# Kernel tuning notes

Measured on AMD Instinct MI355X. Metric: run time of the kernel, lower is better.

The kernel has to match this reference:

```python
import jax, jax.numpy as jnp
import numpy as np

PATCH = 288
DIM = 2048
SCALE = DIM ** -0.5
NUM_INSTANCE = 4
B, Q, H, W = 32, 16, 24, 12


def _layernorm(x):
    # elementwise_affine=False LayerNorm, eps=1e-5
    m = jnp.mean(x, axis=-1, keepdims=True)
    v = jnp.mean((x - m) ** 2, axis=-1, keepdims=True)
    return (x - m) / jnp.sqrt(v + 1e-5)


def _l2norm(x):
    n = jnp.sqrt(jnp.sum(x * x, axis=-1, keepdims=True))
    return x / jnp.maximum(n, 1e-12)


def _catcher(x, g, cam_embed, Wq, Wg, pos_embed):
    # x: [B,Q,C] queries; g: [B,N,C] tokens; cam_embed: [B*N//PATCH,1,C] or None
    rel_q = jnp.einsum('bqc,dc->bqd', x, Wq)
    Bg, N, C = g.shape
    G = Bg * N // PATCH
    g2 = g.reshape(G, PATCH, C)
    rel = _l2norm(g2)
    rel = jax.nn.softmax(jnp.einsum('gpc,gqc->gpq', rel, rel), axis=-1)
    g2 = jnp.einsum('gpq,gqc->gpc', rel, g2)  # [G,PATCH,C]
    if cam_embed is not None:
        rel_g = g2 + cam_embed.reshape(G, 1, C)  # cam embed replaces pos embed (as in torch)
    else:
        rel_g = g2 + pos_embed
    g_out = g2.reshape(Bg, N, C)
    rel_g = jnp.einsum('bnc,dc->bnd', rel_g.reshape(Bg, N, C), Wg)
    att = jax.nn.softmax(jnp.einsum('bqc,bnc->bqn', rel_q, rel_g) * SCALE, axis=-1)
    out = jnp.einsum('bqn,bnc->bqc', att, g_out)
    return out, att


def _deltaor(x, g, Wq, Wg):
    q = _layernorm(x)
    rel_q = jnp.einsum('bqc,dc->bqd', q, Wq)
    g = g - jnp.mean(x, axis=1, keepdims=True)
    g = _layernorm(g)
    rel_g = jnp.einsum('bnc,dc->bnd', g, Wg)
    att = jax.nn.softmax(jnp.einsum('bqc,bnc->bqn', rel_q, rel_g) * SCALE, axis=-1)
    return x + jnp.einsum('bqn,bnc->bqc', att, g)


def setup_inputs() -> dict:
    key = jax.random.key(0)
    ks = jax.random.split(key, 12)
    w_scale = DIM ** -0.5
    return {
        'x': jax.random.normal(ks[0], (B, DIM, H, W), dtype=jnp.float32),
        'cam_ids': jax.random.randint(ks[1], (B,), 1, 7),
        'sub': jax.random.randint(ks[2], (B,), 0, 2).astype(bool),
        'query_v': 0.02 * jax.random.normal(ks[3], (1, Q, DIM), dtype=jnp.float32),
        'prototype': 0.02 * jax.random.normal(ks[4], (1, 2048, DIM), dtype=jnp.float32),
        'weights': jnp.ones((1, Q, 1), dtype=jnp.float32),
        'cam_table': 0.02 * jax.random.normal(ks[5], (6, 1, DIM), dtype=jnp.float32),
        'pos_embed': 0.02 * jax.random.normal(ks[6], (1, PATCH, DIM), dtype=jnp.float32),
        'Wcq': w_scale * jax.random.normal(ks[7], (DIM, DIM), dtype=jnp.float32),
        'Wcg': w_scale * jax.random.normal(ks[8], (DIM, DIM), dtype=jnp.float32),
        'Wdq': w_scale * jax.random.normal(ks[9], (DIM, DIM), dtype=jnp.float32),
        'Wdg': w_scale * jax.random.normal(ks[10], (DIM, DIM), dtype=jnp.float32),
    }


def reference(x, cam_ids, sub, query_v, prototype, weights, cam_table, pos_embed,
              Wcq, Wcg, Wdq, Wdg):
    Bx, C, Hx, Wx = x.shape
    HW = Hx * Wx
    xs = jnp.transpose(x.reshape(Bx, C, HW), (0, 2, 1))  # [B,HW,C]
    query = jnp.broadcast_to(query_v, (Bx,) + query_v.shape[1:])
    proto = jnp.broadcast_to(prototype, (Bx,) + prototype.shape[1:])
    cam_embed = cam_table[cam_ids - 1]  # [B,1,C]

    f_rel, _ = _catcher(query, xs, cam_embed, Wcq, Wcg, pos_embed)
    f_pro = _deltaor(f_rel, proto, Wdq, Wdg)

    # training branch (P2R shares weights with Q2R)
    f_rec, _ = _catcher(f_pro, xs, cam_embed, Wcq, Wcg, pos_embed)

    G = Bx // NUM_INSTANCE
    ce = cam_embed.reshape(G, 1, NUM_INSTANCE, 1, C)
    ce = jnp.broadcast_to(ce, (G, NUM_INSTANCE, NUM_INSTANCE, 1, C)).reshape(Bx, NUM_INSTANCE, C)
    xr = xs.reshape(G, 1, NUM_INSTANCE, HW, C)
    xr = jnp.broadcast_to(xr, (G, NUM_INSTANCE, NUM_INSTANCE, HW, C)).reshape(Bx, NUM_INSTANCE * HW, C)
    # torch.cat([a[~sub], a[sub]]) == stable sort by sub (False first)
    perm = jnp.argsort(sub.astype(jnp.int32))
    ce = ce[perm]
    xr = xr[perm]
    f_cor, _ = _catcher(f_pro, xr, ce, Wcq, Wcg, pos_embed)

    f_pro = jax.nn.softmax(weights, axis=1) * f_pro
    return f_rel, f_pro, f_rec, f_cor
```

## Files before the change

### kernel.cpp

```cpp
#include <hip/hip_runtime.h>
#include <math.h>

static constexpr float SCALE = 0.022097086912079612f;

typedef __bf16 bf16x4 __attribute__((ext_vector_type(4)));
typedef __bf16 bf16x8 __attribute__((ext_vector_type(8)));
typedef float  f32x4  __attribute__((ext_vector_type(4)));

__device__ __forceinline__ float wred_sum(float v){
  #pragma unroll
  for (int o=32;o>0;o>>=1) v += __shfl_down(v,o,64);
  return v;
}
__device__ __forceinline__ float wred_max(float v){
  #pragma unroll
  for (int o=32;o>0;o>>=1) v = fmaxf(v, __shfl_down(v,o,64));
  return v;
}
__device__ __forceinline__ float block_sum(float v, float* red){
  int tid=threadIdx.x, w=tid>>6, l=tid&63, nw=(int)(blockDim.x>>6);
  v = wred_sum(v);
  __syncthreads();
  if (l==0) red[w]=v;
  __syncthreads();
  float r=0.f;
  for (int i=0;i<nw;i++) r += red[i];
  return r;
}
__device__ __forceinline__ float block_max(float v, float* red){
  int tid=threadIdx.x, w=tid>>6, l=tid&63, nw=(int)(blockDim.x>>6);
  v = wred_max(v);
  __syncthreads();
  if (l==0) red[w]=v;
  __syncthreads();
  float r=red[0];
  for (int i=1;i<nw;i++) r = fmaxf(r, red[i]);
  return r;
}

template<int MT, int NT, int WM, int WN>
__global__ __launch_bounds__(256, 2)
void gemm_nt_mfma(float* __restrict__ Cm, const float* __restrict__ Am,
                  const float* __restrict__ Bm, int M, int N, int K,
                  int lda, int ldb, int ldc, long sA, long sB, long sC,
                  float alpha, const int* __restrict__ browidx, long sBrow,
                  int KS, float* __restrict__ Part)
{
  constexpr int BM = MT*16*WM;
  constexpr int BN = NT*16*WN;
  constexpr int LDH = 40;
  constexpr int AST = (BM+31)/32;
  constexpr int BST = (BN+31)/32;
  __shared__ __bf16 Ah[BM*LDH];
  __shared__ __bf16 Al[BM*LDH];
  __shared__ __bf16 Bh[BN*LDH];
  __shared__ __bf16 Bl[BN*LDH];
  int ZZ = gridDim.z / KS;
  int z  = blockIdx.z % ZZ;
  int ks = blockIdx.z / ZZ;
  const float* A = Am + (long)z*sA;
  const float* B = Bm + (long)z*sB;
  float* C = Cm + (long)z*sC;
  const bool useB = (browidx != nullptr);
  const int* brow = useB ? (browidx + (long)z*sBrow) : nullptr;
  int Kc = ((K + KS*32 - 1) / (KS*32)) * 32;
  int kbeg = ks*Kc;
  int kend = min(K, kbeg + Kc);
  int m0 = blockIdx.y*BM, n0 = blockIdx.x*BN;
  int t = threadIdx.x;
  int srow = t>>3, skoff = (t&7)*4;

  float4 areg[AST], breg[BST];
  auto loadAB = [&](int k0){
    #pragma unroll
    for (int s=0;s<AST;++s){
      int row = srow + 32*s; int gm = m0+row;
      areg[s] = make_float4(0.f,0.f,0.f,0.f);
      if (row < BM && gm < M) areg[s] = *(const float4*)(A + (long)gm*lda + k0 + skoff);
    }
    #pragma unroll
    for (int s=0;s<BST;++s){
      int row = srow + 32*s; int gn = n0+row;
      breg[s] = make_float4(0.f,0.f,0.f,0.f);
      if (row < BN && gn < N){
        long r = useB ? (long)brow[gn] : (long)gn;
        breg[s] = *(const float4*)(B + r*ldb + k0 + skoff);
      }
    }
  };
  auto writeLDS = [&](){
    #pragma unroll
    for (int s=0;s<AST;++s){
      int row = srow + 32*s;
      if (row < BM){
        float vv[4] = {areg[s].x, areg[s].y, areg[s].z, areg[s].w};
        bf16x4 hv, lv;
        #pragma unroll
        for (int e=0;e<4;++e){
          __bf16 h = (__bf16)vv[e];
          hv[e] = h;
          lv[e] = (__bf16)(vv[e] - (float)h);
        }
        *(bf16x4*)&Ah[row*LDH + skoff] = hv;
        *(bf16x4*)&Al[row*LDH + skoff] = lv;
      }
    }
    #pragma unroll
    for (int s=0;s<BST;++s){
      int row = srow + 32*s;
      if (row < BN){
        float vv[4] = {breg[s].x, breg[s].y, breg[s].z, breg[s].w};
        bf16x4 hv, lv;
        #pragma unroll
        for (int e=0;e<4;++e){
          __bf16 h = (__bf16)vv[e];
          hv[e] = h;
          lv[e] = (__bf16)(vv[e] - (float)h);
        }
        *(bf16x4*)&Bh[row*LDH + skoff] = hv;
        *(bf16x4*)&Bl[row*LDH + skoff] = lv;
      }
    }
  };

  int lane = t & 63, wid = t >> 6;
  int wm = (WM==1) ? 0 : (wid / WN);
  int wn = wid % WN;
  int mw = wm*MT*16, nw = wn*NT*16;
  int fr = lane & 15, fq = (lane>>4)*8;

  f32x4 acc[MT][NT];
  #pragma unroll
  for (int i=0;i<MT;++i)
    #pragma unroll
    for (int j=0;j<NT;++j) acc[i][j] = (f32x4){0.f,0.f,0.f,0.f};

  if (kbeg < kend) loadAB(kbeg);
  for (int k0=kbeg; k0<kend; k0+=32){
    writeLDS();
    __syncthreads();
    if (k0+32 < kend) loadAB(k0+32);
    bf16x8 ah[MT], al[MT], bh[NT], bl[NT];
    #pragma unroll
    for (int i=0;i<MT;++i){
      ah[i] = *(const bf16x8*)&Ah[(mw+i*16+fr)*LDH + fq];
      al[i] = *(const bf16x8*)&Al[(mw+i*16+fr)*LDH + fq];
    }
    #pragma unroll
    for (int j=0;j<NT;++j){
      bh[j] = *(const bf16x8*)&Bh[(nw+j*16+fr)*LDH + fq];
      bl[j] = *(const bf16x8*)&Bl[(nw+j*16+fr)*LDH + fq];
    }
    #pragma unroll
    for (int i=0;i<MT;++i)
      #pragma unroll
      for (int j=0;j<NT;++j){
        acc[i][j] = __builtin_amdgcn_mfma_f32_16x16x32_bf16(ah[i], bh[j], acc[i][j], 0,0,0);
        acc[i][j] = __builtin_amdgcn_mfma_f32_16x16x32_bf16(ah[i], bl[j], acc[i][j], 0,0,0);
        acc[i][j] = __builtin_amdgcn_mfma_f32_16x16x32_bf16(al[i], bh[j], acc[i][j], 0,0,0);
      }
    __syncthreads();
  }
  float wf = (KS==1) ? alpha : 1.f;
  float* Cw = C; int ldw = ldc;
  if (ks > 0){ Cw = Part + ((long)(ks-1)*ZZ + z)*(long)M*N; ldw = N; }
  int er = (lane>>4)*4, ec = lane & 15;
  #pragma unroll
  for (int i=0;i<MT;++i){
    int mbase = m0 + mw + i*16 + er;
    #pragma unroll
    for (int r=0;r<4;++r){
      int mm = mbase + r;
      if (mm < M){
        long cro = (long)mm*ldw;
        #pragma unroll
        for (int j=0;j<NT;++j){
          int nn = n0 + nw + j*16 + ec;
          if (nn < N) Cw[cro + nn] = wf*acc[i][j][r];
        }
      }
    }
  }
}

template<int MT, int NT, int WM, int WN>
__global__ __launch_bounds__(256, 2)
void gemm_nt_bs(float* __restrict__ C,
                const __bf16* __restrict__ Ahg, const __bf16* __restrict__ Alg,
                const __bf16* __restrict__ Bhg, const __bf16* __restrict__ Blg,
                int M, int N, int K, int lda, int ldb, int ldc,
                float alpha, int KS, float* __restrict__ Part)
{
  constexpr int BM = MT*16*WM;
  constexpr int BN = NT*16*WN;
  constexpr int LDH = 40;
  __shared__ __bf16 Ah[BM*LDH];
  __shared__ __bf16 Al[BM*LDH];
  __shared__ __bf16 Bh[BN*LDH];
  __shared__ __bf16 Bl[BN*LDH];
  int ks = blockIdx.z;
  int Kc = ((K + KS*32 - 1) / (KS*32)) * 32;
  int kbeg = ks*Kc;
  int kend = min(K, kbeg + Kc);
  int m0 = blockIdx.y*BM, n0 = blockIdx.x*BN;
  int t = threadIdx.x;
  constexpr int ASl = (BM*4 + 255)/256;
  constexpr int BSl = (BN*4 + 255)/256;
  bf16x8 arh[ASl], arl[ASl], brh[BSl], brl[BSl];
  bf16x8 zed;
  #pragma unroll
  for (int e=0;e<8;++e) zed[e] = (__bf16)0.f;

  auto loadAB = [&](int k0){
    #pragma unroll
    for (int i=0;i<ASl;++i){
      int s = t + 256*i;
      arh[i] = zed; arl[i] = zed;
      if (s < BM*4){
        int row = s>>2, koff = (s&3)*8; int gm = m0+row;
        if (gm < M){
          long off = (long)gm*lda + k0 + koff;
          arh[i] = *(const bf16x8*)(Ahg + off);
          arl[i] = *(const bf16x8*)(Alg + off);
        }
      }
    }
    #pragma unroll
    for (int i=0;i<BSl;++i){
      int s = t + 256*i;
      brh[i] = zed; brl[i] = zed;
      if (s < BN*4){
        int row = s>>2, koff = (s&3)*8; int gn = n0+row;
        if (gn < N){
          long off = (long)gn*ldb + k0 + koff;
          brh[i] = *(const bf16x8*)(Bhg + off);
          brl[i] = *(const bf16x8*)(Blg + off);
        }
      }
    }
  };
  auto writeLDS = [&](){
    #pragma unroll
    for (int i=0;i<ASl;++i){
      int s = t + 256*i;
      if (s < BM*4){
        int row = s>>2, koff = (s&3)*8;
        *(bf16x8*)&Ah[row*LDH + koff] = arh[i];
        *(bf16x8*)&Al[row*LDH + koff] = arl[i];
      }
    }
    #pragma unroll
    for (int i=0;i<BSl;++i){
      int s = t + 256*i;
      if (s < BN*4){
        int row = s>>2, koff = (s&3)*8;
        *(bf16x8*)&Bh[row*LDH + koff] = brh[i];
        *(bf16x8*)&Bl[row*LDH + koff] = brl[i];
      }
    }
  };

  int lane = t & 63, wid = t >> 6;
  int wm = (WM==1) ? 0 : (wid / WN);
  int wn = wid % WN;
  int mw = wm*MT*16, nw = wn*NT*16;
  int fr = lane & 15, fq = (lane>>4)*8;

  f32x4 acc[MT][NT];
  #pragma unroll
  for (int i=0;i<MT;++i)
    #pragma unroll
    for (int j=0;j<NT;++j) acc[i][j] = (f32x4){0.f,0.f,0.f,0.f};

  if (kbeg < kend) loadAB(kbeg);
  for (int k0=kbeg; k0<kend; k0+=32){
    writeLDS();
    __syncthreads();
    if (k0+32 < kend) loadAB(k0+32);
    bf16x8 ah[MT], al[MT], bh[NT], bl[NT];
    #pragma unroll
    for (int i=0;i<MT;++i){
      ah[i] = *(const bf16x8*)&Ah[(mw+i*16+fr)*LDH + fq];
      al[i] = *(const bf16x8*)&Al[(mw+i*16+fr)*LDH + fq];
    }
    #pragma unroll
    for (int j=0;j<NT;++j){
      bh[j] = *(const bf16x8*)&Bh[(nw+j*16+fr)*LDH + fq];
      bl[j] = *(const bf16x8*)&Bl[(nw+j*16+fr)*LDH + fq];
    }
    #pragma unroll
    for (int i=0;i<MT;++i)
      #pragma unroll
      for (int j=0;j<NT;++j){
        acc[i][j] = __builtin_amdgcn_mfma_f32_16x16x32_bf16(ah[i], bh[j], acc[i][j], 0,0,0);
        acc[i][j] = __builtin_amdgcn_mfma_f32_16x16x32_bf16(ah[i], bl[j], acc[i][j], 0,0,0);
        acc[i][j] = __builtin_amdgcn_mfma_f32_16x16x32_bf16(al[i], bh[j], acc[i][j], 0,0,0);
      }
    __syncthreads();
  }
  float wf = (KS==1) ? alpha : 1.f;
  float* Cw = C; int ldw = ldc;
  if (ks > 0){ Cw = Part + (long)(ks-1)*(long)M*N; ldw = N; }
  int er = (lane>>4)*4, ec = lane & 15;
  #pragma unroll
  for (int i=0;i<MT;++i){
    int mbase = m0 + mw + i*16 + er;
    #pragma unroll
    for (int r=0;r<4;++r){
      int mm = mbase + r;
      if (mm < M){
        long cro = (long)mm*ldw;
        #pragma unroll
        for (int j=0;j<NT;++j){
          int nn = n0 + nw + j*16 + ec;
          if (nn < N) Cw[cro + nn] = wf*acc[i][j][r];
        }
      }
    }
  }
}

__global__ __launch_bounds__(256) void k_reduce(float* __restrict__ C, const float* __restrict__ Part,
                                                long total, int S, float alpha){
  for (long i = (long)blockIdx.x*blockDim.x + threadIdx.x; i < total;
       i += (long)gridDim.x*blockDim.x){
    float v = C[i];
    for (int s=0;s<S;++s) v += Part[(long)s*total + i];
    C[i] = alpha*v;
  }
}

__global__ __launch_bounds__(256) void k_reduce_split(float* __restrict__ C, const float* __restrict__ Part,
                                                      long total, int S, float alpha,
                                                      __bf16* __restrict__ H, __bf16* __restrict__ L){
  long n4 = total >> 2;
  for (long i = (long)blockIdx.x*blockDim.x + threadIdx.x; i < n4;
       i += (long)gridDim.x*blockDim.x){
    float4 v = ((float4*)C)[i];
    for (int s=0;s<S;++s){
      float4 p = ((const float4*)(Part + (long)s*total))[i];
      v.x += p.x; v.y += p.y; v.z += p.z; v.w += p.w;
    }
    v.x *= alpha; v.y *= alpha; v.z *= alpha; v.w *= alpha;
    ((float4*)C)[i] = v;
    float vv[4] = {v.x, v.y, v.z, v.w};
    bf16x4 h, l;
    #pragma unroll
    for (int e=0;e<4;++e){
      __bf16 hh = (__bf16)vv[e];
      h[e] = hh;
      l[e] = (__bf16)(vv[e] - (float)hh);
    }
    ((bf16x4*)H)[i] = h;
    ((bf16x4*)L)[i] = l;
  }
}

__global__ __launch_bounds__(256) void k_split(const float* __restrict__ X,
                                               __bf16* __restrict__ H, __bf16* __restrict__ L, long n){
  long n4 = n >> 2;
  for (long i = (long)blockIdx.x*blockDim.x + threadIdx.x; i < n4;
       i += (long)gridDim.x*blockDim.x){
    float4 v = ((const float4*)X)[i];
    float vv[4] = {v.x, v.y, v.z, v.w};
    bf16x4 h, l;
    #pragma unroll
    for (int e=0;e<4;++e){
      __bf16 hh = (__bf16)vv[e];
      h[e] = hh;
      l[e] = (__bf16)(vv[e] - (float)hh);
    }
    ((bf16x4*)H)[i] = h;
    ((bf16x4*)L)[i] = l;
  }
}

__global__ __launch_bounds__(256, 2) void k_pv(
    float* __restrict__ C, float* __restrict__ Part,
    const float* __restrict__ Pm, long sP, int K, int Kc,
    const float* __restrict__ G, long sG, const int* __restrict__ SB)
{
  extern __shared__ float Pl[];
  int b = blockIdx.y, ks = blockIdx.z;
  int kbeg = ks * Kc;
  int kend = min(K, kbeg + Kc);
  int len = kend - kbeg;
  int c0 = blockIdx.x*1024 + threadIdx.x*4;
  const float* Pb = Pm + (long)b*sP;
  for (int i = threadIdx.x; i < 16*len; i += 256){
    int q = i / len, kk = i - q*len;
    Pl[q*Kc + kk] = Pb[(long)q*K + kbeg + kk];
  }
  __syncthreads();
  f32x4 acc[16];
  #pragma unroll
  for (int q=0;q<16;++q) acc[q] = (f32x4){0.f,0.f,0.f,0.f};
  int kk = 0;
  while (kk < len){
    int kg = kbeg + kk;
    int seg = kg / 288;
    int row = kg - seg*288;
    int nrow = min(288 - row, len - kk);
    const float* gp = (SB ? (G + (long)SB[(b<<2)+seg]*sG) : (G + (long)b*sG))
                      + (long)row*2048 + c0;
    for (int r = 0; r < nrow; r += 4, kk += 4){
      f32x4 g0 = *(const f32x4*)(gp);
      f32x4 g1 = *(const f32x4*)(gp + 2048);
      f32x4 g2 = *(const f32x4*)(gp + 4096);
      f32x4 g3 = *(const f32x4*)(gp + 6144);
      gp += 8192;
      #pragma unroll
      for (int q=0;q<16;++q){
        f32x4 p = *(const f32x4*)&Pl[q*Kc + kk];
        acc[q] += p[0]*g0;
        acc[q] += p[1]*g1;
        acc[q] += p[2]*g2;
        acc[q] += p[3]*g3;
      }
    }
  }
  float* Cw = (ks==0) ? C : (Part + (long)(ks-1)*1048576);
  long obase = (long)b*32768 + c0;
  #pragma unroll
  for (int q=0;q<16;++q) *(f32x4*)&Cw[obase + (long)q*2048] = acc[q];
}

__global__ void k_tr(const float* __restrict__ in, float* __restrict__ out, int R, int C){
  __shared__ float tile[32][33];
  long zo = (long)blockIdx.z * R * C;
  int r0 = blockIdx.y*32, c0 = blockIdx.x*32;
  int tx = threadIdx.x, ty = threadIdx.y;
  #pragma unroll
  for (int j=0;j<32;j+=8)
    tile[ty+j][tx] = in[zo + (long)(r0+ty+j)*C + c0+tx];
  __syncthreads();
  #pragma unroll
  for (int j=0;j<32;j+=8)
    out[zo + (long)(c0+ty+j)*R + r0+tx] = tile[tx][ty+j];
}

__global__ void k_tr_split(const float* __restrict__ in, __bf16* __restrict__ oh,
                           __bf16* __restrict__ ol, int R, int C){
  __shared__ float tile[32][33];
  int r0 = blockIdx.y*32, c0 = blockIdx.x*32;
  int tx = threadIdx.x, ty = threadIdx.y;
  #pragma unroll
  for (int j=0;j<32;j+=8)
    tile[ty+j][tx] = in[(long)(r0+ty+j)*C + c0+tx];
  __syncthreads();
  #pragma unroll
  for (int j=0;j<32;j+=8){
    float v = tile[tx][ty+j];
    __bf16 h = (__bf16)v;
    long idx = (long)(c0+ty+j)*R + r0+tx;
    oh[idx] = h;
    ol[idx] = (__bf16)(v - (float)h);
  }
}

__global__ __launch_bounds__(256) void k_rowstats(const float* __restrict__ X, long ldx, int cols,
                                                  float* __restrict__ mu, float* __restrict__ m2){
  int r = blockIdx.x;
  const float* row = X + (long)r*ldx;
  float s=0.f, s2=0.f;
  for (int c = threadIdx.x*4; c < cols; c += 1024){
    float4 v = *(const float4*)(row+c);
    s  += v.x+v.y+v.z+v.w;
    s2 += v.x*v.x+v.y*v.y+v.z*v.z+v.w*v.w;
  }
  __shared__ float red[8];
  s  = block_sum(s,  red);
  s2 = block_sum(s2, red);
  if (threadIdx.x==0){ mu[r]=s/(float)cols; m2[r]=s2; }
}

__global__ __launch_bounds__(256) void k_softmax_gram(float* __restrict__ S, const float* __restrict__ Part,
                                                      const float* __restrict__ m2xs){
  int r = blockIdx.x;
  int b = r / 288, p = r % 288;
  float* row = S + (long)r * 288;
  const float* prow = Part + (long)b*82944 + (long)p*288;
  const float* m2 = m2xs + (long)b*288;
  float rp = 1.f / fmaxf(sqrtf(m2[p]), 1e-12f);
  int tid = threadIdx.x;
  __shared__ float red[8];
  float lv[2];
  #pragma unroll
  for (int i=0;i<2;++i){
    int q = tid + i*256;
    lv[i] = (q<288) ? (row[q]+prow[q])*rp/fmaxf(sqrtf(m2[q]),1e-12f) : -1e30f;
  }
  float mx = fmaxf(lv[0], lv[1]);
  mx = block_max(mx, red);
  float s = 0.f;
  #pragma unroll
  for (int i=0;i<2;++i){
    int q = tid + i*256;
    float e = (q<288) ? expf(lv[i]-mx) : 0.f;
    lv[i]=e; s+=e;
  }
  s = block_sum(s, red);
  float inv = 1.f/s;
  #pragma unroll
  for (int i=0;i<2;++i){ int q = tid + i*256; if (q<288) row[q]=lv[i]*inv; }
}

__global__ __launch_bounds__(256) void k_softmax_plain_r(float* __restrict__ X,
// ... 111 lines not shown
  int r = blockIdx.x; int b = r >> 4;
  const float* a = relq2 + (long)r*2048;
  const float* m = Mx + (long)b*2048;
  float s=0.f, sw=0.f;
  for (int c = threadIdx.x*4; c < 2048; c += 1024){
    float4 va=*(const float4*)(a+c), vm=*(const float4*)(m+c), vw=*(const float4*)(muw+c);
    s  += va.x*vm.x+va.y*vm.y+va.z*vm.z+va.w*vm.w;
    sw += va.x*vw.x+va.y*vw.y+va.z*vw.z+va.w*vw.w;
  }
  __shared__ float red[8];
  s  = block_sum(s,  red);
  sw = block_sum(sw, red);
  if (threadIdx.x==0){ qm[r]=s; qw[r]=sw; }
}

__global__ __launch_bounds__(256) void k_score2_s(const float* __restrict__ QPw, const float* __restrict__ qm,
                                                  const float* __restrict__ qw,
                                                  const float* __restrict__ sigma, const float* __restrict__ mu_p,
                                                  __bf16* __restrict__ QH, __bf16* __restrict__ QL,
                                                  float* __restrict__ W1, float* __restrict__ Wmu, float scale){
  int r = blockIdx.x; int b = r >> 4;
  const float* row = QPw + (long)r*2048;
  const float* sg = sigma + (long)b*2048;
  int tid = threadIdx.x;
  __shared__ float red[8];
  float qmr = qm[r];
  float qwr2048 = 2048.f * qw[r];
  float lv[8], ls[8], lmp[8];
  #pragma unroll
  for (int i=0;i<8;++i){
    int n = tid + i*256;
    float sgn = sg[n];
    float mpn = mu_p[n];
    ls[i] = sgn;
    lmp[i] = mpn;
    lv[i] = scale * (row[n] - qwr2048*mpn - qmr) / sgn;
  }
  float mx = -1e30f;
  #pragma unroll
  for (int i=0;i<8;++i) mx = fmaxf(mx, lv[i]);
  mx = block_max(mx, red);
  float se=0.f, sw=0.f, swm=0.f;
  #pragma unroll
  for (int i=0;i<8;++i){
    float e = expf(lv[i]-mx);
    lv[i] = e; se += e;
    float wv = e/ls[i];
    sw += wv; swm += wv*lmp[i];
  }
  se  = block_sum(se,  red);
  sw  = block_sum(sw,  red);
  swm = block_sum(swm, red);
  float inv = 1.f/se;
  #pragma unroll
  for (int i=0;i<8;++i){
    int n = tid + i*256;
    float v = lv[i]*inv/ls[i];
    __bf16 h = (__bf16)v;
    long idx = (long)r*2048 + n;
    QH[idx] = h;
    QL[idx] = (__bf16)(v - (float)h);
  }
  if (tid==0){ W1[r]=sw*inv; Wmu[r]=swm*inv; }
}

__global__ void k_fpro_final_s(const float* __restrict__ frel, const float* __restrict__ out2,
                               const float* __restrict__ meanx, const float* __restrict__ mu_m,
                               const float* __restrict__ W1, const float* __restrict__ Wmu,
                               const float* __restrict__ wsm,
                               __bf16* __restrict__ FH, __bf16* __restrict__ FL,
                               float* __restrict__ fout){
  int r = blockIdx.y; int c = blockIdx.x*256 + threadIdx.x;
  int b = r >> 4, q = r & 15;
  long idx = (long)r*2048 + c;
  float w1 = W1[r];
  float v = frel[idx] + out2[idx] - meanx[(long)b*2048+c]*w1 - Wmu[r] + mu_m[b]*w1;
  __bf16 h = (__bf16)v;
  FH[idx] = h;
  FL[idx] = (__bf16)(v - (float)h);
  fout[idx] = wsm[q] * v;
}

__global__ void k_camb(const float* __restrict__ cam_table, const int* __restrict__ cam_ids,
                       float* __restrict__ camb){
  int b = blockIdx.y; int c = blockIdx.x*256 + threadIdx.x;
  camb[(long)b*2048 + c] = cam_table[(long)(cam_ids[b]-1)*2048 + c];
}

__global__ void k_wsoft(const float* __restrict__ w, float* __restrict__ wsm){
  if (threadIdx.x==0){
    float mx=-1e30f;
    for (int i=0;i<16;++i) mx=fmaxf(mx,w[i]);
    float e[16], s=0.f;
    for (int i=0;i<16;++i){ e[i]=expf(w[i]-mx); s+=e[i]; }
    for (int i=0;i<16;++i) wsm[i]=e[i]/s;
  }
}

__global__ void k_perm(const void* __restrict__ subp, int* __restrict__ gidx, int* __restrict__ SB){
  __shared__ int perm[32];
  if (threadIdx.x==0){
    const int* pi = (const int*)subp;
    const float* pf = (const float*)subp;
    const unsigned char* pb = (const unsigned char*)subp;
    int sv[32]; bool okI=true, okF=true;
    for (int i=0;i<32;++i){ int v=pi[i]; if (v!=0 && v!=1) okI=false; }
    for (int i=0;i<32;++i){ float f=pf[i]; if (f!=0.f && f!=1.f) okF=false; }
    for (int i=0;i<32;++i){
      if (okI) sv[i]=pi[i];
      else if (okF) sv[i]=(pf[i]!=0.f)?1:0;
      else sv[i]=(pb[i]!=0)?1:0;
    }
    int pos=0;
    for (int i=0;i<32;++i) if (!sv[i]) perm[pos++]=i;
    for (int i=0;i<32;++i) if ( sv[i]) perm[pos++]=i;
  }
  __syncthreads();
  for (int i = threadIdx.x; i < 128; i += blockDim.x){
    int b = i>>2, j = i&3;
    SB[i] = ((perm[b]>>2)<<2) + j;
  }
  for (int idx = threadIdx.x; idx < 32*1152; idx += blockDim.x){
    int b = idx / 1152, rem = idx % 1152, j = rem / 288, n = rem % 288;
    int src = ((perm[b] >> 2) << 2) + j;
    gidx[idx] = src*288 + n;
  }
}

extern "C" void kernel_launch(void* const* d_in, const int* in_sizes, int n_in,
                              void* d_out, int out_size, void* d_ws, size_t ws_size,
                              hipStream_t stream) {
  const float* x        = (const float*)d_in[0];
  const int*   cam_ids  = (const int*)d_in[1];
  const void*  subp     = d_in[2];
  const float* query_v  = (const float*)d_in[3];
  const float* proto    = (const float*)d_in[4];
  const float* weights  = (const float*)d_in[5];
  const float* cam_tab  = (const float*)d_in[6];
  const float* Wcq      = (const float*)d_in[8];
  const float* Wcg      = (const float*)d_in[9];
  const float* Wdq      = (const float*)d_in[10];
  const float* Wdg      = (const float*)d_in[11];
  float* out = (float*)d_out;
  float* ws  = (float*)d_ws;

  size_t o = 0;
  float* S     = ws + o; o += 2654208;
  __bf16* QLNh   = (__bf16*)S;
  __bf16* QLNl   = (__bf16*)(S + 524288);
  __bf16* RELQ2h = (__bf16*)(S + 1048576);
  __bf16* RELQ2l = (__bf16*)(S + 1572864);
  float* XSR   = ws + o; o += 18874368;
  float* XS    = XSR;
  float* PART  = XSR;
  __bf16* WCQh  = (__bf16*)(XSR + 6291456);
  __bf16* WCQl  = (__bf16*)(XSR + 8388608);
  __bf16* WCGTh = (__bf16*)(XSR + 10485760);
  __bf16* WCGTl = (__bf16*)(XSR + 12582912);
  __bf16* ROTh  = (__bf16*)(XSR + 14680064);
  __bf16* ROTl  = (__bf16*)(XSR + 16777216);
  float* GMIX  = ws + o; o += 18874368;
  float* MU_XS = ws + o; o += 9216;
  float* M2_XS = ws + o; o += 9216;
  float* CAMB  = ws + o; o += 65536;
  float* RQ0   = ws + o; o += 32768;
  float* RQW   = ws + o; o += 32768;
  float* SREL  = ws + o; o += 147456;
  float* MU_FR = ws + o; o += 512;
  float* M2_FR = ws + o; o += 512;
  float* T1    = ws + o; o += 1048576;
  float* RELQ2 = ws + o; o += 1048576;
  float* MEANX = ws + o; o += 65536;
  float* MU_P  = ws + o; o += 2048;
  float* M2_P  = ws + o; o += 2048;
  float* MU_M  = ws + o; o += 64;
  float* M2_M  = ws + o; o += 64;
  float* MU_W  = ws + o; o += 2048;
  float* M2_W  = ws + o; o += 2048;
  float* PM    = ws + o; o += 65536;
  float* SIGMA = ws + o; o += 65536;
  float* MX    = ws + o; o += 65536;
  float* QP    = ws + o; o += 1048576;
  float* QM    = ws + o; o += 512;
  float* QW    = ws + o; o += 512;
  float* W1    = ws + o; o += 512;
  float* WMU   = ws + o; o += 512;
  float* OUT2  = ws + o; o += 1048576;
  __bf16* FPROh = (__bf16*)(ws + o);
  __bf16* FPROl = (__bf16*)(ws + o + 524288); o += 1048576;
  float* RQ2   = ws + o; o += 1048576;
  float* RQW2  = ws + o; o += 1048576;
  float* SREC  = ws + o; o += 147456;
  float* SCOR  = ws + o; o += 589824;
  float* CC    = ws + o; o += 16384;
  float* WSM   = ws + o; o += 16;
  __bf16* T1h   = (__bf16*)(ws + o);
  __bf16* T1l   = (__bf16*)(ws + o + 524288); o += 1048576;
  __bf16* QPWh  = (__bf16*)(ws + o);
  __bf16* QPWl  = (__bf16*)(ws + o + 524288); o += 1048576;
  __bf16* RQ2h  = (__bf16*)(ws + o);
  __bf16* RQ2l  = (__bf16*)(ws + o + 524288); o += 1048576;
  __bf16* QVh   = (__bf16*)(ws + o);
  __bf16* QVl   = (__bf16*)(ws + o + 16384); o += 32768;
  __bf16* RQ0h  = (__bf16*)(ws + o);
  __bf16* RQ0l  = (__bf16*)(ws + o + 16384); o += 32768;
  int*   GIDX  = (int*)(ws + o); o += 36864;
  int*   SB    = (int*)(ws + o); o += 128;

  float* F_REL = out;
  float* F_PRO = out + 1048576;
  float* F_REC = out + 2097152;
  float* F_COR = out + 3145728;

  float* PART_CC = PART + 4000000;

  k_tr<<<dim3(9,64,32), dim3(32,8), 0, stream>>>(x, XS, 2048, 288);
  k_rowstats<<<9216, 256, 0, stream>>>(XS, 2048, 2048, MU_XS, M2_XS);
  gemm_nt_mfma<3,3,2,2><<<dim3(3,3,64), 256, 0, stream>>>(S, XS, XS, 288,288,2048,
      2048,2048,288, 589824,589824,82944, 1.f, nullptr,0, 2, GMIX);
  k_softmax_gram<<<9216, 256, 0, stream>>>(S, GMIX, M2_XS);
  gemm_nt_mfma<3,4,2,2><<<dim3(16,3,32), 256, 0, stream>>>(GMIX, S, x, 288,2048,288,
      288,288,2048, 82944,589824,589824, 1.f, nullptr,0, 1, nullptr);
  k_split<<<2048, 256, 0, stream>>>(Wcq, WCQh, WCQl, 4194304L);
  k_tr_split<<<dim3(64,64), dim3(32,8), 0, stream>>>(Wcg, WCGTh, WCGTl, 2048, 2048);
  k_split<<<32, 256, 0, stream>>>(query_v, QVh, QVl, 32768L);
  k_camb<<<dim3(8,32), 256, 0, stream>>>(cam_tab, cam_ids, CAMB);
  k_perm<<<1, 256, 0, stream>>>(subp, GIDX, SB);
  k_wsoft<<<1, 64, 0, stream>>>(weights, WSM);

  gemm_nt_bs<1,4,1,4><<<dim3(8,1,16), 256, 0, stream>>>(RQ0, QVh,QVl, WCQh,WCQl,
      16,2048,2048, 2048,2048,2048, 1.f, 16, PART);
  k_reduce_split<<<64, 256, 0, stream>>>(RQ0, PART, 32768L, 15, 1.f, RQ0h, RQ0l);
  gemm_nt_bs<1,4,1,4><<<dim3(8,1,16), 256, 0, stream>>>(RQW, RQ0h,RQ0l, WCGTh,WCGTl,
      16,2048,2048, 2048,2048,2048, 1.f, 16, PART);
  k_reduce<<<64, 256, 0, stream>>>(RQW, PART, 32768L, 15, 1.f);
  gemm_nt_mfma<1,4,1,4><<<dim3(2,1,256), 256, 0, stream>>>(SREL, RQW, GMIX, 16,288,2048,
      2048,2048,288, 0,589824,4608, SCALE, nullptr,0, 8, PART);
  k_softmax_plain_r<<<512, 256, 0, stream>>>(SREL, PART, 7, SCALE);
  k_pv<<<dim3(2,32,7), 256, 16*44*4, stream>>>(F_REL, PART, SREL, 4608, 288, 44,
      GMIX, 589824, nullptr);
  k_reduce<<<1024, 256, 0, stream>>>(F_REL, PART, 1048576L, 6, 1.f);

  k_rowstats<<<512, 256, 0, stream>>>(F_REL, 2048, 2048, MU_FR, M2_FR);
  k_ln_apply_s<<<dim3(8,512), 256, 0, stream>>>(F_REL, MU_FR, M2_FR, QLNh, QLNl);
  k_meanx<<<dim3(8,32), 256, 0, stream>>>(F_REL, MEANX);
  k_rowstats<<<32,   256, 0, stream>>>(MEANX, 2048, 2048, MU_M, M2_M);
  k_rowstats<<<2048, 256, 0, stream>>>(proto, 2048, 2048, MU_P, M2_P);
  k_rowstats<<<2048, 256, 0, stream>>>(Wdg,   2048, 2048, MU_W, M2_W);
  k_split<<<2048, 256, 0, stream>>>(Wdq, ROTh, ROTl, 4194304L);
  gemm_nt_bs<2,2,2,2><<<dim3(32,8,3), 256, 0, stream>>>(RELQ2, QLNh,QLNl, ROTh,ROTl,
      512,2048,2048, 2048,2048,2048, 1.f, 3, PART);
  k_reduce_split<<<1024, 256, 0, stream>>>(RELQ2, PART, 1048576L, 2, 1.f, RELQ2h, RELQ2l);
  gemm_nt_mfma<1,4,1,4><<<dim3(8,2,8), 256, 0, stream>>>(PM, MEANX, proto, 32,2048,2048,
      2048,2048,2048, 0,0,0, 1.f, nullptr,0, 8, PART);
  k_reduce<<<256, 256, 0, stream>>>(PM, PART, 65536L, 7, 1.f);
  k_sigma<<<dim3(8,32), 256, 0, stream>>>(PM, MU_P, M2_P, MU_M, M2_M, SIGMA);
  k_tr_split<<<dim3(64,64), dim3(32,8), 0, stream>>>(Wdg, ROTh, ROTl, 2048, 2048);
  gemm_nt_bs<2,2,2,2><<<dim3(32,8,3), 256, 0, stream>>>(T1, RELQ2h,RELQ2l, ROTh,ROTl,
      512,2048,2048, 2048,2048,2048, 1.f, 3, PART);
  k_reduce_split<<<1024, 256, 0, stream>>>(T1, PART, 1048576L, 2, 1.f, T1h, T1l);
  gemm_nt_mfma<1,4,1,4><<<dim3(8,2,8), 256, 0, stream>>>(MX, MEANX, Wdg, 32,2048,2048,
      2048,2048,2048, 0,0,0, 1.f, nullptr,0, 8, PART);
  k_reduce<<<256, 256, 0, stream>>>(MX, PART, 65536L, 7, 1.f);
  k_fixrow<<<dim3(8,32), 256, 0, stream>>>(MX, MU_M, MU_W);
  k_split<<<2048, 256, 0, stream>>>(proto, ROTh, ROTl, 4194304L);
  gemm_nt_bs<2,2,2,2><<<dim3(32,8,3), 256, 0, stream>>>(QP, T1h,T1l, ROTh,ROTl,
      512,2048,2048, 2048,2048,2048, 1.f, 3, PART);
  k_reduce<<<1024, 256, 0, stream>>>(QP, PART, 1048576L, 2, 1.f);
  k_qm2<<<512, 256, 0, stream>>>(RELQ2, MX, MU_W, QM, QW);
  k_score2_s<<<512, 256, 0, stream>>>(QP, QM, QW, SIGMA, MU_P, QPWh, QPWl, W1, WMU, SCALE);
  k_tr_split<<<dim3(64,64), dim3(32,8), 0, stream>>>(proto, ROTh, ROTl, 2048, 2048);
  gemm_nt_bs<2,2,2,2><<<dim3(32,8,3), 256, 0, stream>>>(OUT2, QPWh,QPWl, ROTh,ROTl,
      512,2048,2048, 2048,2048,2048, 1.f, 3, PART);
  k_reduce<<<1024, 256, 0, stream>>>(OUT2, PART, 1048576L, 2, 1.f);
  k_fpro_final_s<<<dim3(8,512), 256, 0, stream>>>(F_REL, OUT2, MEANX, MU_M, W1, WMU, WSM,
                                                  FPROh, FPROl, F_PRO);

  gemm_nt_bs<2,2,2,2><<<dim3(32,8,3), 256, 0, stream>>>(RQ2, FPROh,FPROl, WCQh,WCQl,
      512,2048,2048, 2048,2048,2048, 1.f, 3, PART);
  k_reduce_split<<<1024, 256, 0, stream>>>(RQ2, PART, 1048576L, 2, 1.f, RQ2h, RQ2l);
  gemm_nt_bs<2,2,2,2><<<dim3(32,8,3), 256, 0, stream>>>(RQW2, RQ2h,RQ2l, WCGTh,WCGTl,
      512,2048,2048, 2048,2048,2048, 1.f, 3, PART);
  k_reduce<<<1024, 256, 0, stream>>>(RQW2, PART, 1048576L, 2, 1.f);
  gemm_nt_mfma<1,4,1,4><<<dim3(2,1,256), 256, 0, stream>>>(SREC, RQW2, GMIX, 16,288,2048,
      2048,2048,288, 32768,589824,4608, SCALE, nullptr,0, 8, PART);
  k_softmax_plain_r<<<512, 256, 0, stream>>>(SREC, PART, 7, SCALE);
  k_pv<<<dim3(2,32,7), 256, 16*44*4, stream>>>(F_REC, PART, SREC, 4608, 288, 44,
      GMIX, 589824, nullptr);
  k_reduce<<<1024, 256, 0, stream>>>(F_REC, PART, 1048576L, 6, 1.f);

  gemm_nt_mfma<1,4,1,4><<<dim3(1,32,8), 256, 0, stream>>>(CC, RQW2, CAMB, 512,32,2048,
      2048,2048,32, 0,0,0, 1.f, nullptr,0, 8, PART_CC);
  gemm_nt_mfma<1,4,1,4><<<dim3(5,1,128), 256, 0, stream>>>(SCOR, RQW2, GMIX, 16,1152,2048,
      2048,2048,1152, 32768,0,18432, SCALE, GIDX,1152, 4, PART);
  k_softmax_seg<<<512, 256, 0, stream>>>(SCOR, PART, 3, CC, PART_CC, 7, SB, SCALE);
  k_pv<<<dim3(2,32,7), 256, 16*168*4, stream>>>(F_COR, PART, SCOR, 18432, 1152, 168,
      GMIX, 589824, SB);
  k_reduce<<<1024, 256, 0, stream>>>(F_COR, PART, 1048576L, 6, 1.f);
}
```

Measured before the change: 972.5 us.

## Store GMIX as pre-split bf16 hi/lo and use split-bf16 GEMMs for score stages

The mixing GEMM epilogue now writes GMIX directly as bf16 high/low halves instead of fp32. The score GEMMs against GMIX and CAMB switch to a batched, row-gathered split-bf16 GEMM that reads pre-split operands instead of splitting fp32 tiles at load time. The PV kernel reads the bf16 pairs and reconstructs fp32, using a 2-wide column tile with register prefetch and twice as many blocks. This reduces per-tile conversion work, at the cost of an extra pass to split the query-side operands and a hi+lo approximation of the fp32 values.

```diff
diff --git a/kernel.cpp b/kernel.cpp
--- a/kernel.cpp
+++ b/kernel.cpp
@@ -3,8 +3,10 @@
 
 static constexpr float SCALE = 0.022097086912079612f;
 
+typedef __bf16 bf16x2 __attribute__((ext_vector_type(2)));
 typedef __bf16 bf16x4 __attribute__((ext_vector_type(4)));
 typedef __bf16 bf16x8 __attribute__((ext_vector_type(8)));
+typedef float  f32x2  __attribute__((ext_vector_type(2)));
 typedef float  f32x4  __attribute__((ext_vector_type(4)));
 
 __device__ __forceinline__ float wred_sum(float v){
@@ -44,7 +46,8 @@
                   const float* __restrict__ Bm, int M, int N, int K,
                   int lda, int ldb, int ldc, long sA, long sB, long sC,
                   float alpha, const int* __restrict__ browidx, long sBrow,
-                  int KS, float* __restrict__ Part)
+                  int KS, float* __restrict__ Part,
+                  __bf16* __restrict__ Chp, __bf16* __restrict__ Clp)
 {
   constexpr int BM = MT*16*WM;
   constexpr int BN = NT*16*WN;
@@ -176,7 +179,17 @@
         #pragma unroll
         for (int j=0;j<NT;++j){
           int nn = n0 + nw + j*16 + ec;
-          if (nn < N) Cw[cro + nn] = wf*acc[i][j][r];
+          if (nn < N){
+            float v = wf*acc[i][j][r];
+            if (Chp){
+              long po = (long)z*sC + cro + nn;
+              __bf16 h = (__bf16)v;
+              Chp[po] = h;
+              Clp[po] = (__bf16)(v - (float)h);
+            } else {
+              Cw[cro + nn] = v;
+            }
+          }
         }
       }
     }
@@ -185,11 +198,13 @@
 
 template<int MT, int NT, int WM, int WN>
 __global__ __launch_bounds__(256, 2)
-void gemm_nt_bs(float* __restrict__ C,
-                const __bf16* __restrict__ Ahg, const __bf16* __restrict__ Alg,
-                const __bf16* __restrict__ Bhg, const __bf16* __restrict__ Blg,
-                int M, int N, int K, int lda, int ldb, int ldc,
-                float alpha, int KS, float* __restrict__ Part)
+void gemm_nt_bsg(float* __restrict__ Cm,
+                 const __bf16* __restrict__ Ahg, const __bf16* __restrict__ Alg,
+                 const __bf16* __restrict__ Bhg, const __bf16* __restrict__ Blg,
+                 int M, int N, int K, int lda, int ldb, int ldc,
+                 long sA, long sB, long sC,
+                 float alpha, const int* __restrict__ browidx, long sBrow,
+                 int KS, float* __restrict__ Part)
 {
   constexpr int BM = MT*16*WM;
   constexpr int BN = NT*16*WN;
@@ -198,7 +213,16 @@
   __shared__ __bf16 Al[BM*LDH];
   __shared__ __bf16 Bh[BN*LDH];
   __shared__ __bf16 Bl[BN*LDH];
-  int ks = blockIdx.z;
+  int ZZ = gridDim.z / KS;
+  int z  = blockIdx.z % ZZ;
+  int ks = blockIdx.z / ZZ;
+  const __bf16* Ahb = Ahg + (long)z*sA;
+  const __bf16* Alb = Alg + (long)z*sA;
+  const __bf16* Bhb = Bhg + (long)z*sB;
+  const __bf16* Blb = Blg + (long)z*sB;
+  float* C = Cm + (long)z*sC;
+  const bool useB = (browidx != nullptr);
+  const int* brow = useB ? (browidx + (long)z*sBrow) : nullptr;
   int Kc = ((K + KS*32 - 1) / (KS*32)) * 32;
   int kbeg = ks*Kc;
   int kend = min(K, kbeg + Kc);
@@ -220,8 +244,8 @@
         int row = s>>2, koff = (s&3)*8; int gm = m0+row;
         if (gm < M){
           long off = (long)gm*lda + k0 + koff;
-          arh[i] = *(const bf16x8*)(Ahg + off);
-          arl[i] = *(const bf16x8*)(Alg + off);
+          arh[i] = *(const bf16x8*)(Ahb + off);
+          arl[i] = *(const bf16x8*)(Alb + off);
         }
       }
     }
@@ -232,9 +256,10 @@
       if (s < BN*4){
         int row = s>>2, koff = (s&3)*8; int gn = n0+row;
         if (gn < N){
-          long off = (long)gn*ldb + k0 + koff;
-          brh[i] = *(const bf16x8*)(Bhg + off);
-          brl[i] = *(const bf16x8*)(Blg + off);
+          long r = useB ? (long)brow[gn] : (long)gn;
+          long off = r*ldb + k0 + koff;
+          brh[i] = *(const bf16x8*)(Bhb + off);
+          brl[i] = *(const bf16x8*)(Blb + off);
         }
       }
     }
@@ -300,7 +325,7 @@
   }
   float wf = (KS==1) ? alpha : 1.f;
   float* Cw = C; int ldw = ldc;
-  if (ks > 0){ Cw = Part + (long)(ks-1)*(long)M*N; ldw = N; }
+  if (ks > 0){ Cw = Part + ((long)(ks-1)*ZZ + z)*(long)M*N; ldw = N; }
   int er = (lane>>4)*4, ec = lane & 15;
   #pragma unroll
   for (int i=0;i<MT;++i){
@@ -375,40 +400,56 @@
   }
 }
 
-__global__ __launch_bounds__(256, 2) void k_pv(
+__global__ __launch_bounds__(256, 2) void k_pv2(
     float* __restrict__ C, float* __restrict__ Part,
     const float* __restrict__ Pm, long sP, int K, int Kc,
-    const float* __restrict__ G, long sG, const int* __restrict__ SB)
+    const __bf16* __restrict__ Gh, const __bf16* __restrict__ Gl,
+    long sG, const int* __restrict__ SB)
 {
   extern __shared__ float Pl[];
   int b = blockIdx.y, ks = blockIdx.z;
   int kbeg = ks * Kc;
   int kend = min(K, kbeg + Kc);
   int len = kend - kbeg;
-  int c0 = blockIdx.x*1024 + threadIdx.x*4;
+  int c0 = blockIdx.x*512 + threadIdx.x*2;
   const float* Pb = Pm + (long)b*sP;
   for (int i = threadIdx.x; i < 16*len; i += 256){
     int q = i / len, kk = i - q*len;
     Pl[q*Kc + kk] = Pb[(long)q*K + kbeg + kk];
   }
   __syncthreads();
-  f32x4 acc[16];
-  #pragma unroll
-  for (int q=0;q<16;++q) acc[q] = (f32x4){0.f,0.f,0.f,0.f};
+  f32x2 acc[16];
+  #pragma unroll
+  for (int q=0;q<16;++q) acc[q] = (f32x2){0.f,0.f};
   int kk = 0;
   while (kk < len){
     int kg = kbeg + kk;
     int seg = kg / 288;
     int row = kg - seg*288;
     int nrow = min(288 - row, len - kk);
-    const float* gp = (SB ? (G + (long)SB[(b<<2)+seg]*sG) : (G + (long)b*sG))
-                      + (long)row*2048 + c0;
+    long base = (SB ? (long)SB[(b<<2)+seg]*sG : (long)b*sG) + (long)row*2048 + c0;
+    const __bf16* gh = Gh + base;
+    const __bf16* gl = Gl + base;
+    bf16x2 h0,h1,h2,h3,l0,l1,l2,l3;
+    h0 = *(const bf16x2*)(gh);       l0 = *(const bf16x2*)(gl);
+    h1 = *(const bf16x2*)(gh+2048);  l1 = *(const bf16x2*)(gl+2048);
+    h2 = *(const bf16x2*)(gh+4096);  l2 = *(const bf16x2*)(gl+4096);
+    h3 = *(const bf16x2*)(gh+6144);  l3 = *(const bf16x2*)(gl+6144);
+    gh += 8192; gl += 8192;
     for (int r = 0; r < nrow; r += 4, kk += 4){
-      f32x4 g0 = *(const f32x4*)(gp);
-      f32x4 g1 = *(const f32x4*)(gp + 2048);
-      f32x4 g2 = *(const f32x4*)(gp + 4096);
-      f32x4 g3 = *(const f32x4*)(gp + 6144);
-      gp += 8192;
+      bf16x2 nh0=h0,nh1=h1,nh2=h2,nh3=h3,nl0=l0,nl1=l1,nl2=l2,nl3=l3;
+      if (r + 4 < nrow){
+        nh0 = *(const bf16x2*)(gh);       nl0 = *(const bf16x2*)(gl);
+        nh1 = *(const bf16x2*)(gh+2048);  nl1 = *(const bf16x2*)(gl+2048);
+        nh2 = *(const bf16x2*)(gh+4096);  nl2 = *(const bf16x2*)(gl+4096);
+        nh3 = *(const bf16x2*)(gh+6144);  nl3 = *(const bf16x2*)(gl+6144);
+        gh += 8192; gl += 8192;
+      }
+      f32x2 g0, g1, g2, g3;
+      g0[0]=(float)h0[0]+(float)l0[0]; g0[1]=(float)h0[1]+(float)l0[1];
+      g1[0]=(float)h1[0]+(float)l1[0]; g1[1]=(float)h1[1]+(float)l1[1];
+      g2[0]=(float)h2[0]+(float)l2[0]; g2[1]=(float)h2[1]+(float)l2[1];
+      g3[0]=(float)h3[0]+(float)l3[0]; g3[1]=(float)h3[1]+(float)l3[1];
       #pragma unroll
       for (int q=0;q<16;++q){
         f32x4 p = *(const f32x4*)&Pl[q*Kc + kk];
@@ -417,12 +458,14 @@
         acc[q] += p[2]*g2;
         acc[q] += p[3]*g3;
       }
+      h0=nh0; h1=nh1; h2=nh2; h3=nh3;
+      l0=nl0; l1=nl1; l2=nl2; l3=nl3;
     }
   }
   float* Cw = (ks==0) ? C : (Part + (long)(ks-1)*1048576);
   long obase = (long)b*32768 + c0;
   #pragma unroll
-  for (int q=0;q<16;++q) *(f32x4*)&Cw[obase + (long)q*2048] = acc[q];
+  for (int q=0;q<16;++q) *(f32x2*)&Cw[obase + (long)q*2048] = acc[q];
 }
 
 __global__ void k_tr(const float* __restrict__ in, float* __restrict__ out, int R, int C){
@@ -700,9 +743,13 @@
 }
 
 __global__ void k_camb(const float* __restrict__ cam_table, const int* __restrict__ cam_ids,
-                       float* __restrict__ camb){
+                       __bf16* __restrict__ H, __bf16* __restrict__ L){
   int b = blockIdx.y; int c = blockIdx.x*256 + threadIdx.x;
-  camb[(long)b*2048 + c] = cam_table[(long)(cam_ids[b]-1)*2048 + c];
+  float v = cam_table[(long)(cam_ids[b]-1)*2048 + c];
+  __bf16 h = (__bf16)v;
+  long idx = (long)b*2048 + c;
+  H[idx] = h;
+  L[idx] = (__bf16)(v - (float)h);
 }
 
 __global__ void k_wsoft(const float* __restrict__ w, float* __restrict__ wsm){
@@ -777,10 +824,14 @@
   __bf16* WCGTl = (__bf16*)(XSR + 12582912);
   __bf16* ROTh  = (__bf16*)(XSR + 14680064);
   __bf16* ROTl  = (__bf16*)(XSR + 16777216);
-  float* GMIX  = ws + o; o += 18874368;
+  float* GMIXR = ws + o; o += 18874368;
+  __bf16* GMIXh = (__bf16*)GMIXR;
+  __bf16* GMIXl = GMIXh + 18874368;
   float* MU_XS = ws + o; o += 9216;
   float* M2_XS = ws + o; o += 9216;
   float* CAMB  = ws + o; o += 65536;
+  __bf16* CAMBh = (__bf16*)CAMB;
+  __bf16* CAMBl = CAMBh + 65536;
   float* RQ0   = ws + o; o += 32768;
   float* RQW   = ws + o; o += 32768;
   float* SREL  = ws + o; o += 147456;
@@ -808,6 +859,8 @@
   __bf16* FPROl = (__bf16*)(ws + o + 524288); o += 1048576;
   float* RQ2   = ws + o; o += 1048576;
   float* RQW2  = ws + o; o += 1048576;
+  __bf16* RQW2h = (__bf16*)(ws + o);
+  __bf16* RQW2l = RQW2h + 1048576; o += 1048576;
   float* SREC  = ws + o; o += 147456;
   float* SCOR  = ws + o; o += 589824;
   float* CC    = ws + o; o += 16384;
@@ -822,6 +875,8 @@
   __bf16* QVl   = (__bf16*)(ws + o + 16384); o += 32768;
   __bf16* RQ0h  = (__bf16*)(ws + o);
   __bf16* RQ0l  = (__bf16*)(ws + o + 16384); o += 32768;
+  __bf16* RQWh  = (__bf16*)(ws + o);
+  __bf16* RQWl  = RQWh + 32768; o += 32768;
   int*   GIDX  = (int*)(ws + o); o += 36864;
   int*   SB    = (int*)(ws + o); o += 128;
 
@@ -835,28 +890,28 @@
   k_tr<<<dim3(9,64,32), dim3(32,8), 0, stream>>>(x, XS, 2048, 288);
   k_rowstats<<<9216, 256, 0, stream>>>(XS, 2048, 2048, MU_XS, M2_XS);
   gemm_nt_mfma<3,3,2,2><<<dim3(3,3,64), 256, 0, stream>>>(S, XS, XS, 288,288,2048,
-      2048,2048,288, 589824,589824,82944, 1.f, nullptr,0, 2, GMIX);
-  k_softmax_gram<<<9216, 256, 0, stream>>>(S, GMIX, M2_XS);
-  gemm_nt_mfma<3,4,2,2><<<dim3(16,3,32), 256, 0, stream>>>(GMIX, S, x, 288,2048,288,
-      288,288,2048, 82944,589824,589824, 1.f, nullptr,0, 1, nullptr);
+      2048,2048,288, 589824,589824,82944, 1.f, nullptr,0, 2, GMIXR, nullptr, nullptr);
+  k_softmax_gram<<<9216, 256, 0, stream>>>(S, GMIXR, M2_XS);
+  gemm_nt_mfma<3,4,2,2><<<dim3(16,3,32), 256, 0, stream>>>(GMIXR, S, x, 288,2048,288,
+      288,288,2048, 82944,589824,589824, 1.f, nullptr,0, 1, nullptr, GMIXh, GMIXl);
   k_split<<<2048, 256, 0, stream>>>(Wcq, WCQh, WCQl, 4194304L);
   k_tr_split<<<dim3(64,64), dim3(32,8), 0, stream>>>(Wcg, WCGTh, WCGTl, 2048, 2048);
   k_split<<<32, 256, 0, stream>>>(query_v, QVh, QVl, 32768L);
-  k_camb<<<dim3(8,32), 256, 0, stream>>>(cam_tab, cam_ids, CAMB);
+  k_camb<<<dim3(8,32), 256, 0, stream>>>(cam_tab, cam_ids, CAMBh, CAMBl);
   k_perm<<<1, 256, 0, stream>>>(subp, GIDX, SB);
   k_wsoft<<<1, 64, 0, stream>>>(weights, WSM);
 
-  gemm_nt_bs<1,4,1,4><<<dim3(8,1,16), 256, 0, stream>>>(RQ0, QVh,QVl, WCQh,WCQl,
-      16,2048,2048, 2048,2048,2048, 1.f, 16, PART);
+  gemm_nt_bsg<1,4,1,4><<<dim3(8,1,16), 256, 0, stream>>>(RQ0, QVh,QVl, WCQh,WCQl,
+      16,2048,2048, 2048,2048,2048, 0,0,0, 1.f, nullptr,0, 16, PART);
   k_reduce_split<<<64, 256, 0, stream>>>(RQ0, PART, 32768L, 15, 1.f, RQ0h, RQ0l);
-  gemm_nt_bs<1,4,1,4><<<dim3(8,1,16), 256, 0, stream>>>(RQW, RQ0h,RQ0l, WCGTh,WCGTl,
-      16,2048,2048, 2048,2048,2048, 1.f, 16, PART);
-  k_reduce<<<64, 256, 0, stream>>>(RQW, PART, 32768L, 15, 1.f);
-  gemm_nt_mfma<1,4,1,4><<<dim3(2,1,256), 256, 0, stream>>>(SREL, RQW, GMIX, 16,288,2048,
-      2048,2048,288, 0,589824,4608, SCALE, nullptr,0, 8, PART);
+  gemm_nt_bsg<1,4,1,4><<<dim3(8,1,16), 256, 0, stream>>>(RQW, RQ0h,RQ0l, WCGTh,WCGTl,
+      16,2048,2048, 2048,2048,2048, 0,0,0, 1.f, nullptr,0, 16, PART);
+  k_reduce_split<<<64, 256, 0, stream>>>(RQW, PART, 32768L, 15, 1.f, RQWh, RQWl);
+  gemm_nt_bsg<1,4,1,4><<<dim3(2,1,256), 256, 0, stream>>>(SREL, RQWh,RQWl, GMIXh,GMIXl,
+      16,288,2048, 2048,2048,288, 0,589824,4608, SCALE, nullptr,0, 8, PART);
   k_softmax_plain_r<<<512, 256, 0, stream>>>(SREL, PART, 7, SCALE);
-  k_pv<<<dim3(2,32,7), 256, 16*44*4, stream>>>(F_REL, PART, SREL, 4608, 288, 44,
-      GMIX, 589824, nullptr);
+  k_pv2<<<dim3(4,32,7), 256, 16*44*4, stream>>>(F_REL, PART, SREL, 4608, 288, 44,
+      GMIXh, GMIXl, 589824, nullptr);
   k_reduce<<<1024, 256, 0, stream>>>(F_REL, PART, 1048576L, 6, 1.f);
 
   k_rowstats<<<512, 256, 0, stream>>>(F_REL, 2048, 2048, MU_FR, M2_FR);
@@ -866,53 +921,53 @@
   k_rowstats<<<2048, 256, 0, stream>>>(proto, 2048, 2048, MU_P, M2_P);
   k_rowstats<<<2048, 256, 0, stream>>>(Wdg,   2048, 2048, MU_W, M2_W);
   k_split<<<2048, 256, 0, stream>>>(Wdq, ROTh, ROTl, 4194304L);
-  gemm_nt_bs<2,2,2,2><<<dim3(32,8,3), 256, 0, stream>>>(RELQ2, QLNh,QLNl, ROTh,ROTl,
-      512,2048,2048, 2048,2048,2048, 1.f, 3, PART);
+  gemm_nt_bsg<2,2,2,2><<<dim3(32,8,3), 256, 0, stream>>>(RELQ2, QLNh,QLNl, ROTh,ROTl,
+      512,2048,2048, 2048,2048,2048, 0,0,0, 1.f, nullptr,0, 3, PART);
   k_reduce_split<<<1024, 256, 0, stream>>>(RELQ2, PART, 1048576L, 2, 1.f, RELQ2h, RELQ2l);
   gemm_nt_mfma<1,4,1,4><<<dim3(8,2,8), 256, 0, stream>>>(PM, MEANX, proto, 32,2048,2048,
-      2048,2048,2048, 0,0,0, 1.f, nullptr,0, 8, PART);
+      2048,2048,2048, 0,0,0, 1.f, nullptr,0, 8, PART, nullptr, nullptr);
   k_reduce<<<256, 256, 0, stream>>>(PM, PART, 65536L, 7, 1.f);
   k_sigma<<<dim3(8,32), 256, 0, stream>>>(PM, MU_P, M2_P, MU_M, M2_M, SIGMA);
   k_tr_split<<<dim3(64,64), dim3(32,8), 0, stream>>>(Wdg, ROTh, ROTl, 2048, 2048);
-  gemm_nt_bs<2,2,2,2><<<dim3(32,8,3), 256, 0, stream>>>(T1, RELQ2h,RELQ2l, ROTh,ROTl,
-      512,2048,2048, 2048,2048,2048, 1.f, 3, PART);
+  gemm_nt_bsg<2,2,2,2><<<dim3(32,8,3), 256, 0, stream>>>(T1, RELQ2h,RELQ2l, ROTh,ROTl,
+      512,2048,2048, 2048,2048,2048, 0,0,0, 1.f, nullptr,0, 3, PART);
   k_reduce_split<<<1024, 256, 0, stream>>>(T1, PART, 1048576L, 2, 1.f, T1h, T1l);
   gemm_nt_mfma<1,4,1,4><<<dim3(8,2,8), 256, 0, stream>>>(MX, MEANX, Wdg, 32,2048,2048,
-      2048,2048,2048, 0,0,0, 1.f, nullptr,0, 8, PART);
+      2048,2048,2048, 0,0,0, 1.f, nullptr,0, 8, PART, nullptr, nullptr);
   k_reduce<<<256, 256, 0, stream>>>(MX, PART, 65536L, 7, 1.f);
   k_fixrow<<<dim3(8,32), 256, 0, stream>>>(MX, MU_M, MU_W);
   k_split<<<2048, 256, 0, stream>>>(proto, ROTh, ROTl, 4194304L);
-  gemm_nt_bs<2,2,2,2><<<dim3(32,8,3), 256, 0, stream>>>(QP, T1h,T1l, ROTh,ROTl,
-      512,2048,2048, 2048,2048,2048, 1.f, 3, PART);
+  gemm_nt_bsg<2,2,2,2><<<dim3(32,8,3), 256, 0, stream>>>(QP, T1h,T1l, ROTh,ROTl,
+      512,2048,2048, 2048,2048,2048, 0,0,0, 1.f, nullptr,0, 3, PART);
   k_reduce<<<1024, 256, 0, stream>>>(QP, PART, 1048576L, 2, 1.f);
   k_qm2<<<512, 256, 0, stream>>>(RELQ2, MX, MU_W, QM, QW);
   k_score2_s<<<512, 256, 0, stream>>>(QP, QM, QW, SIGMA, MU_P, QPWh, QPWl, W1, WMU, SCALE);
   k_tr_split<<<dim3(64,64), dim3(32,8), 0, stream>>>(proto, ROTh, ROTl, 2048, 2048);
-  gemm_nt_bs<2,2,2,2><<<dim3(32,8,3), 256, 0, stream>>>(OUT2, QPWh,QPWl, ROTh,ROTl,
-      512,2048,2048, 2048,2048,2048, 1.f, 3, PART);
+  gemm_nt_bsg<2,2,2,2><<<dim3(32,8,3), 256, 0, stream>>>(OUT2, QPWh,QPWl, ROTh,ROTl,
+      512,2048,2048, 2048,2048,2048, 0,0,0, 1.f, nullptr,0, 3, PART);
   k_reduce<<<1024, 256, 0, stream>>>(OUT2, PART, 1048576L, 2, 1.f);
   k_fpro_final_s<<<dim3(8,512), 256, 0, stream>>>(F_REL, OUT2, MEANX, MU_M, W1, WMU, WSM,
                                                   FPROh, FPROl, F_PRO);
 
-  gemm_nt_bs<2,2,2,2><<<dim3(32,8,3), 256, 0, stream>>>(RQ2, FPROh,FPROl, WCQh,WCQl,
-      512,2048,2048, 2048,2048,2048, 1.f, 3, PART);
+  gemm_nt_bsg<2,2,2,2><<<dim3(32,8,3), 256, 0, stream>>>(RQ2, FPROh,FPROl, WCQh,WCQl,
+      512,2048,2048, 2048,2048,2048, 0,0,0, 1.f, nullptr,0, 3, PART);
   k_reduce_split<<<1024, 256, 0, stream>>>(RQ2, PART, 1048576L, 2, 1.f, RQ2h, RQ2l);
-  gemm_nt_bs<2,2,2,2><<<dim3(32,8,3), 256, 0, stream>>>(RQW2, RQ2h,RQ2l, WCGTh,WCGTl,
-      512,2048,2048, 2048,2048,2048, 1.f, 3, PART);
-  k_reduce<<<1024, 256, 0, stream>>>(RQW2, PART, 1048576L, 2, 1.f);
-  gemm_nt_mfma<1,4,1,4><<<dim3(2,1,256), 256, 0, stream>>>(SREC, RQW2, GMIX, 16,288,2048,
-      2048,2048,288, 32768,589824,4608, SCALE, nullptr,0, 8, PART);
+  gemm_nt_bsg<2,2,2,2><<<dim3(32,8,3), 256, 0, stream>>>(RQW2, RQ2h,RQ2l, WCGTh,WCGTl,
+      512,2048,2048, 2048,2048,2048, 0,0,0, 1.f, nullptr,0, 3, PART);
+  k_reduce_split<<<1024, 256, 0, stream>>>(RQW2, PART, 1048576L, 2, 1.f, RQW2h, RQW2l);
+  gemm_nt_bsg<1,4,1,4><<<dim3(2,1,256), 256, 0, stream>>>(SREC, RQW2h,RQW2l, GMIXh,GMIXl,
+      16,288,2048, 2048,2048,288, 32768,589824,4608, SCALE, nullptr,0, 8, PART);
   k_softmax_plain_r<<<512, 256, 0, stream>>>(SREC, PART, 7, SCALE);
-  k_pv<<<dim3(2,32,7), 256, 16*44*4, stream>>>(F_REC, PART, SREC, 4608, 288, 44,
-      GMIX, 589824, nullptr);
+  k_pv2<<<dim3(4,32,7), 256, 16*44*4, stream>>>(F_REC, PART, SREC, 4608, 288, 44,
+      GMIXh, GMIXl, 589824, nullptr);
   k_reduce<<<1024, 256, 0, stream>>>(F_REC, PART, 1048576L, 6, 1.f);
 
-  gemm_nt_mfma<1,4,1,4><<<dim3(1,32,8), 256, 0, stream>>>(CC, RQW2, CAMB, 512,32,2048,
-      2048,2048,32, 0,0,0, 1.f, nullptr,0, 8, PART_CC);
-  gemm_nt_mfma<1,4,1,4><<<dim3(5,1,128), 256, 0, stream>>>(SCOR, RQW2, GMIX, 16,1152,2048,
-      2048,2048,1152, 32768,0,18432, SCALE, GIDX,1152, 4, PART);
+  gemm_nt_bsg<1,4,1,4><<<dim3(1,32,8), 256, 0, stream>>>(CC, RQW2h,RQW2l, CAMBh,CAMBl,
+      512,32,2048, 2048,2048,32, 0,0,0, 1.f, nullptr,0, 8, PART_CC);
+  gemm_nt_bsg<1,4,1,4><<<dim3(5,1,128), 256, 0, stream>>>(SCOR, RQW2h,RQW2l, GMIXh,GMIXl,
+      16,1152,2048, 2048,2048,1152, 32768,0,18432, SCALE, GIDX,1152, 4, PART);
   k_softmax_seg<<<512, 256, 0, stream>>>(SCOR, PART, 3, CC, PART_CC, 7, SB, SCALE);
-  k_pv<<<dim3(2,32,7), 256, 16*168*4, stream>>>(F_COR, PART, SCOR, 18432, 1152, 168,
-      GMIX, 589824, SB);
+  k_pv2<<<dim3(4,32,7), 256, 16*168*4, stream>>>(F_COR, PART, SCOR, 18432, 1152, 168,
+      GMIXh, GMIXl, 589824, SB);
   k_reduce<<<1024, 256, 0, stream>>>(F_COR, PART, 1048576L, 6, 1.f);
 }
```

New measurement: 984.9 us. About the same (+1.3%).
